# Performance work log

Measured on AMD Instinct MI355X. Metric: run time of the kernel, lower is better.

Reference implementation:

```python
import jax, jax.numpy as jnp
import numpy as np

DIM = 1024
HEADS = 16
HEAD_DIM = DIM // HEADS
MAX_REL = 1024
B, N = 4, 1024


def setup_inputs() -> dict:
    key = jax.random.key(0)
    k1, k2, k3, k4, k5 = jax.random.split(key, 5)
    x = jax.random.normal(k1, (B, N, DIM), dtype=jnp.float32)
    W_qkv = jax.random.normal(k2, (3 * DIM, DIM), dtype=jnp.float32) * 0.02
    W_proj = jax.random.normal(k3, (DIM, DIM), dtype=jnp.float32) * 0.02
    b_proj = jnp.zeros((DIM,), dtype=jnp.float32)
    Er = jax.random.normal(k4, (MAX_REL, HEAD_DIM), dtype=jnp.float32)
    return {"x": x, "W_qkv": W_qkv, "W_proj": W_proj, "b_proj": b_proj, "Er": Er}


def _relative_skew(S_rel):
    # S_rel: [B, H, L, L] -> pad a zero column on the left, reshape, drop first row
    Bb, H, L, _ = S_rel.shape
    S = jnp.pad(S_rel, ((0, 0), (0, 0), (0, 0), (1, 0)))  # [B,H,L,L+1]
    S = S.reshape(Bb, H, L + 1, L)
    return S[:, :, 1:, :]


def reference(x, W_qkv, W_proj, b_proj, Er):
    Bb, Nn, C = x.shape
    scale = HEAD_DIM ** (-0.5)
    qkv = jnp.einsum('bnc,fc->bnf', x, W_qkv)           # [B,N,3C]
    qkv = qkv.reshape(Bb, Nn, 3, HEADS, HEAD_DIM)
    q = jnp.transpose(qkv[:, :, 0], (0, 2, 1, 3))        # [B,H,N,d]
    k = jnp.transpose(qkv[:, :, 1], (0, 2, 1, 3))
    v = jnp.transpose(qkv[:, :, 2], (0, 2, 1, 3))
    content = jnp.einsum('bhnd,bhmd->bhnm', q, k)        # [B,H,N,N]
    er_seq = Er[:Nn]                                     # [N,d]
    rel = jnp.einsum('bhnd,md->bhnm', q, er_seq)         # [B,H,N,N]
    rel = _relative_skew(rel)
    score = (content + rel) * scale
    causal = jnp.triu(jnp.ones((Nn, Nn), dtype=bool), k=1)
    score = jnp.where(causal, -jnp.inf, score)
    probs = jax.nn.softmax(score, axis=-1)
    out = jnp.einsum('bhnm,bhmd->bhnd', probs, v)        # [B,H,N,d]
    out = jnp.transpose(out, (0, 2, 1, 3)).reshape(Bb, Nn, C)
    return jnp.einsum('bnc,oc->bno', out, W_proj) + b_proj
```

## Files before the change

### kernel.cpp

```cpp
#include <hip/hip_runtime.h>
#include <math.h>

#define BATCH 4
#define SEQ   1024
#define DIM_C 1024
#define HEADS 16
#define HDIM  64
#define F3    3072

typedef short bf8 __attribute__((ext_vector_type(8)));
typedef float f32x4 __attribute__((ext_vector_type(4)));

__device__ __forceinline__ ushort f2bf(float f) {
    union { float f; unsigned u; } c; c.f = f;
    unsigned u = c.u + 0x7fffu + ((c.u >> 16) & 1u);
    return (ushort)(u >> 16);
}
__device__ __forceinline__ float bf2f(ushort s) {
    union { unsigned u; float f; } c; c.u = ((unsigned)s) << 16;
    return c.f;
}

__device__ __forceinline__ void stage16(const ushort* g, ushort* l) {
    __builtin_amdgcn_global_load_lds(
        (const __attribute__((address_space(1))) unsigned int*)g,
        (__attribute__((address_space(3))) unsigned int*)l, 16, 0, 0);
}

__global__ __launch_bounds__(256) void cvt_all_kernel(
    const float* __restrict__ x, const float* __restrict__ wqkv,
    const float* __restrict__ wproj, const float* __restrict__ er,
    ushort* __restrict__ xb, ushort* __restrict__ wqkvb,
    ushort* __restrict__ wprojb, ushort* __restrict__ erb)
{
    const int blk = blockIdx.x;
    const float* src; ushort* dst; size_t off;
    if (blk < 2048)      { src = x;     dst = xb;     off = (size_t)blk * 2048; }
    else if (blk < 3584) { src = wqkv;  dst = wqkvb;  off = (size_t)(blk - 2048) * 2048; }
    else if (blk < 4096) { src = wproj; dst = wprojb; off = (size_t)(blk - 3584) * 2048; }
    else                 { src = er;    dst = erb;    off = (size_t)(blk - 4096) * 2048; }
    size_t i = off + (size_t)threadIdx.x * 8;
    float4 v0 = *(const float4*)&src[i];
    float4 v1 = *(const float4*)&src[i + 4];
    ushort o[8];
    o[0] = f2bf(v0.x); o[1] = f2bf(v0.y); o[2] = f2bf(v0.z); o[3] = f2bf(v0.w);
    o[4] = f2bf(v1.x); o[5] = f2bf(v1.y); o[6] = f2bf(v1.z); o[7] = f2bf(v1.w);
    *(uint4*)&dst[i] = *(uint4*)o;
}

__device__ __forceinline__ void gemm_core(
    const ushort* __restrict__ a, const ushort* __restrict__ b,
    ushort* As, ushort* Bs, int m0, int f0, int t, f32x4 (&acc)[4][4])
{
    const int lane = t & 63, w = t >> 6;
    const int lc = lane & 15, g4 = lane >> 4;
    const int wm = (w >> 1) * 64, wn = (w & 1) * 64;
    const int rowS = w * 32 + (lane >> 2);
    const int kkS  = (lane & 3) * 8;

    for (int kt = 0; kt < 32; ++kt) {
        const int k0 = kt * 32;
        __syncthreads();
        #pragma unroll
        for (int ii = 0; ii < 2; ++ii) {
            stage16(&a[(size_t)(m0 + rowS + ii * 16) * 1024 + k0 + kkS],
                    &As[(w * 2 + ii) * 512]);
            stage16(&b[(size_t)(f0 + rowS + ii * 16) * 1024 + k0 + kkS],
                    &Bs[(w * 2 + ii) * 512]);
        }
        __syncthreads();
        bf8 af[4], bfr[4];
        #pragma unroll
        for (int mb = 0; mb < 4; ++mb)
            af[mb] = *(const bf8*)&As[(wm + mb * 16 + lc) * 32 + g4 * 8];
        #pragma unroll
        for (int nb = 0; nb < 4; ++nb)
            bfr[nb] = *(const bf8*)&Bs[(wn + nb * 16 + lc) * 32 + g4 * 8];
        #pragma unroll
        for (int mb = 0; mb < 4; ++mb)
            #pragma unroll
            for (int nb = 0; nb < 4; ++nb)
                acc[mb][nb] = __builtin_amdgcn_mfma_f32_16x16x32_bf16(
                    af[mb], bfr[nb], acc[mb][nb], 0, 0, 0);
    }
}

__global__ __launch_bounds__(256) void gemm_qkv_mfma(
    const ushort* __restrict__ xb, const ushort* __restrict__ wb,
    ushort* __restrict__ qp, ushort* __restrict__ kp, ushort* __restrict__ vp)
{
    __shared__ __align__(16) ushort As[128 * 32];
    __shared__ __align__(16) ushort Bs[128 * 32];
    const int t = threadIdx.x;
    const int m0 = blockIdx.y * 128, f0 = blockIdx.x * 128;
    f32x4 acc[4][4];
    #pragma unroll
    for (int mb = 0; mb < 4; ++mb)
        #pragma unroll
        for (int nb = 0; nb < 4; ++nb) acc[mb][nb] = (f32x4){0.f, 0.f, 0.f, 0.f};

    gemm_core(xb, wb, As, Bs, m0, f0, t, acc);

    const int lane = t & 63, w = t >> 6;
    const int lc = lane & 15, g4 = lane >> 4;
    const int wm = (w >> 1) * 64, wn = (w & 1) * 64;
    const int s = f0 >> 10;
    #pragma unroll
    for (int mb = 0; mb < 4; ++mb)
        #pragma unroll
        for (int nb = 0; nb < 4; ++nb) {
            const int f = f0 + wn + nb * 16 + lc;
            const int h = (f >> 6) & 15, d = f & 63;
            if (s == 2) {
                const int m = m0 + wm + mb * 16 + g4 * 4;
                const int b = m >> 10, n = m & 1023;
                ushort4 o;
                o.x = f2bf(acc[mb][nb][0]); o.y = f2bf(acc[mb][nb][1]);
                o.z = f2bf(acc[mb][nb][2]); o.w = f2bf(acc[mb][nb][3]);
                *(ushort4*)&vp[(((size_t)(b * 16 + h)) * 64 + d) * 1024 + n] = o;
            } else {
                ushort* dst = (s == 0) ? qp : kp;
                #pragma unroll
                for (int i = 0; i < 4; ++i) {
                    const int m = m0 + wm + mb * 16 + g4 * 4 + i;
                    const int b = m >> 10, n = m & 1023;
                    dst[(((size_t)(b * 16 + h)) * 1024 + n) * 64 + d] = f2bf(acc[mb][nb][i]);
                }
            }
        }
}

__global__ __launch_bounds__(256) void gemm_proj_mfma(
    const ushort* __restrict__ ab, const ushort* __restrict__ wb,
    const float* __restrict__ bias, float* __restrict__ y)
{
    __shared__ __align__(16) ushort As[128 * 32];
    __shared__ __align__(16) ushort Bs[128 * 32];
    const int t = threadIdx.x;
    const int m0 = blockIdx.y * 128, f0 = blockIdx.x * 128;
    f32x4 acc[4][4];
    #pragma unroll
    for (int mb = 0; mb < 4; ++mb)
        #pragma unroll
        for (int nb = 0; nb < 4; ++nb) acc[mb][nb] = (f32x4){0.f, 0.f, 0.f, 0.f};

    gemm_core(ab, wb, As, Bs, m0, f0, t, acc);

    const int lane = t & 63, w = t >> 6;
    const int lc = lane & 15, g4 = lane >> 4;
    const int wm = (w >> 1) * 64, wn = (w & 1) * 64;
    #pragma unroll
    for (int mb = 0; mb < 4; ++mb)
        #pragma unroll
        for (int nb = 0; nb < 4; ++nb) {
            const int f = f0 + wn + nb * 16 + lc;
            const float bv = bias[f];
            #pragma unroll
            for (int i = 0; i < 4; ++i) {
                const int m = m0 + wm + mb * 16 + g4 * 4 + i;
                y[(size_t)m * 1024 + f] = acc[mb][nb][i] + bv;
            }
        }
}

__global__ __launch_bounds__(256, 2) void attn_mfma_kernel(
    const ushort* __restrict__ qg, const ushort* __restrict__ kg,
    const ushort* __restrict__ vtg, const ushort* __restrict__ erg,
    ushort* __restrict__ pOd, float* __restrict__ pL)
{
    __shared__ __align__(16) ushort k_s[2][64][64];
    __shared__ __align__(16) ushort vt_s[2][64][64];
    __shared__ __align__(16) ushort e_s[3][64][64];
    __shared__ __align__(16) ushort p_s[4][16][72];

    const int t = threadIdx.x;
    const int w = t >> 6, lane = t & 63;
    const int lc = lane & 15, g4 = lane >> 4;
    const int b = blockIdx.z, h = blockIdx.y;
    const int u = blockIdx.x;
    const int cum[17] = {0,1,2,3,4,6,8,10,12,15,18,21,24,28,32,36,40};
    int bx = 0;
    #pragma unroll
    for (int j = 1; j < 16; ++j) if (u >= cum[j]) bx = j;
    const int part = u - cum[bx];
    const int t0 = part * 4;
    const int t1 = min(t0 + 4, bx + 1);

    const int n0 = bx * 64;
    const int n0w = n0 + w * 16;
    const int ew0 = 48 - 16 * w;
    const int ch0 = 15 - bx + t0;

    const ushort* qb  = qg  + ((size_t)(b * 16 + h)) * 65536;
    const ushort* kb  = kg  + ((size_t)(b * 16 + h)) * 65536;
    const ushort* vtb = vtg + ((size_t)(b * 16 + h)) * 65536;

    const int srow = lane >> 3;
    const int scol = ((lane & 7) ^ (srow & 7)) * 8;
    const int sr0  = w * 16 + srow;
    const int rsw  = (lc & 7) * 8;

    #pragma unroll
    for (int ii = 0; ii < 2; ++ii) {
        stage16(&kb[(size_t)(t0 * 64 + sr0 + ii * 8) * 64 + scol], &k_s[0][w * 16 + ii * 8][0]);
        stage16(&vtb[(size_t)(sr0 + ii * 8) * 1024 + t0 * 64 + scol], &vt_s[0][w * 16 + ii * 8][0]);
    }
    #pragma unroll
    for (int cc = 0; cc < 2; ++cc) {
        const int ch = ch0 + cc;
        #pragma unroll
        for (int ii = 0; ii < 2; ++ii) {
            int gr = ch * 64 + sr0 + ii * 8;
            gr = (gr > 1023) ? 1023 : gr;
            stage16(&erg[(size_t)gr * 64 + scol], &e_s[ch % 3][w * 16 + ii * 8][0]);
        }
    }

    bf8 qf[2];
    #pragma unroll
    for (int c = 0; c < 2; ++c)
        qf[c] = *(const bf8*)&qb[(size_t)(n0w + lc) * 64 + c * 32 + g4 * 8];

    asm volatile("s_waitcnt vmcnt(0)" ::: "memory");
    __builtin_amdgcn_s_barrier();

    const f32x4 z4 = {0.f, 0.f, 0.f, 0.f};
    f32x4 od[4] = {z4, z4, z4, z4};
    float lrow[4] = {0.f, 0.f, 0.f, 0.f};
    int cur = 0;

    for (int tt = t0; tt < t1; ++tt) {
        const int m0 = tt * 64;
        const int ch = 15 - bx + tt;
        const int eB = ch * 64;

        if (tt + 1 < t1) {
            const int m1 = m0 + 64;
            const int nxt = cur ^ 1;
            #pragma unroll
            for (int ii = 0; ii < 2; ++ii) {
                stage16(&kb[(size_t)(m1 + sr0 + ii * 8) * 64 + scol],
                        &k_s[nxt][w * 16 + ii * 8][0]);
                stage16(&vtb[(size_t)(sr0 + ii * 8) * 1024 + m1 + scol],
                        &vt_s[nxt][w * 16 + ii * 8][0]);
            }
            #pragma unroll
            for (int ii = 0; ii < 2; ++ii) {
                int gr = (ch + 2) * 64 + sr0 + ii * 8;
                gr = (gr > 1023) ? 1023 : gr;
                stage16(&erg[(size_t)gr * 64 + scol], &e_s[(ch + 2) % 3][w * 16 + ii * 8][0]);
            }
            asm volatile("s_waitcnt vmcnt(6)" ::: "memory");
        } else {
            asm volatile("s_waitcnt vmcnt(0)" ::: "memory");
        }
        __builtin_amdgcn_s_barrier();

        f32x4 sc[4] = {z4, z4, z4, z4};
        #pragma unroll
        for (int jt = 0; jt < 4; ++jt)
            #pragma unroll
            for (int c = 0; c < 2; ++c) {
                bf8 kf = *(const bf8*)&k_s[cur][jt * 16 + lc][((c * 4 + g4) * 8) ^ rsw];
                sc[jt] = __builtin_amdgcn_mfma_f32_16x16x32_bf16(qf[c], kf, sc[jt], 0, 0, 0);
            }

        f32x4 rc[5] = {z4, z4, z4, z4, z4};
        #pragma unroll
        for (int jr = 0; jr < 5; ++jr) {
            const int g  = eB + ew0 + jr * 16 + lc;
            const int s3 = (g >> 6) % 3;
            const int r  = g & 63;
            #pragma unroll
            for (int c = 0; c < 2; ++c) {
                bf8 ef = *(const bf8*)&e_s[s3][r][((c * 4 + g4) * 8) ^ rsw];
                rc[jr] = __builtin_amdgcn_mfma_f32_16x16x32_bf16(qf[c], ef, rc[jr], 0, 0, 0);
            }
        }

        #pragma unroll
        for (int i = 0; i < 4; ++i) {
            const int row = g4 * 4 + i;
            const int n = n0w + row;
            const int src = (lc + 15 - row) & 15;
            float sh[5];
            #pragma unroll
            for (int jr = 0; jr < 5; ++jr)
                sh[jr] = __shfl(rc[jr][i], src, 16);
            #pragma unroll
            for (int jt = 0; jt < 4; ++jt) {
                const float rel = (lc > row) ? sh[jt + 1] : sh[jt];
                const float s = (sc[jt][i] + rel) * 0.125f;
                const int m = m0 + jt * 16 + lc;
                const float p = (m <= n) ? __expf(s) : 0.f;
                p_s[w][row][jt * 16 + lc] = f2bf(p);
                lrow[i] += p;
            }
        }
        asm volatile("s_waitcnt lgkmcnt(0)" ::: "memory");

        bf8 pf[2];
        #pragma unroll
        for (int c = 0; c < 2; ++c)
            pf[c] = *(const bf8*)&p_s[w][lc][c * 32 + g4 * 8];
        #pragma unroll
        for (int dt = 0; dt < 4; ++dt)
            #pragma unroll
            for (int c = 0; c < 2; ++c) {
                bf8 vf = *(const bf8*)&vt_s[cur][dt * 16 + lc][((c * 4 + g4) * 8) ^ rsw];
                od[dt] = __builtin_amdgcn_mfma_f32_16x16x32_bf16(pf[c], vf, od[dt], 0, 0, 0);
            }

        __builtin_amdgcn_s_barrier();
        cur ^= 1;
    }

    #pragma unroll
    for (int off = 1; off < 16; off <<= 1)
        #pragma unroll
        for (int i = 0; i < 4; ++i)
            lrow[i] += __shfl_xor(lrow[i], off, 16);

    const size_t pbase = (size_t)((b * 16 + h) * 40 + u);
    #pragma unroll
    for (int i = 0; i < 4; ++i) {
        const int nl = w * 16 + g4 * 4 + i;
        #pragma unroll
        for (int dt = 0; dt < 4; ++dt)
            pOd[pbase * 4096 + nl * 64 + dt * 16 + lc] = f2bf(od[dt][i]);
        if (lc == 0) pL[pbase * 64 + nl] = lrow[i];
    }
}

__global__ __launch_bounds__(256) void attn_combine_kernel(
    const ushort* __restrict__ pOd, const float* __restrict__ pL,
    ushort* __restrict__ attnb)
{
    const int tid = blockIdx.x * 256 + threadIdx.x;
    const int d8 = tid & 7;
    const int n  = (tid >> 3) & 1023;
    const int bh = tid >> 13;
    const int bx = n >> 6, nl = n & 63;
    const int cum[17] = {0,1,2,3,4,6,8,10,12,15,18,21,24,28,32,36,40};
    const int u0 = cum[bx], pc = cum[bx + 1] - cum[bx];

    float acc[8] = {0.f, 0.f, 0.f, 0.f, 0.f, 0.f, 0.f, 0.f};
    float lsum = 0.f;
    for (int j = 0; j < pc; ++j) {
        const size_t base = (size_t)(bh * 40 + u0 + j);
        uint4 pv = *(const uint4*)&pOd[base * 4096 + nl * 64 + d8 * 8];
        const ushort* pp = (const ushort*)&pv;
        #pragma unroll
        for (int e = 0; e < 8; ++e) acc[e] += bf2f(pp[e]);
        lsum += pL[base * 64 + nl];
    }
    const float inv = 1.f / lsum;
    ushort o[8];
    #pragma unroll
    for (int e = 0; e < 8; ++e) o[e] = f2bf(acc[e] * inv);
    const int b = bh >> 4, h = bh & 15;
    *(uint4*)&attnb[((size_t)(b * 1024) + n) * 1024 + h * 64 + d8 * 8] = *(uint4*)o;
}

extern "C" void kernel_launch(void* const* d_in, const int* in_sizes, int n_in,
                              void* d_out, int out_size, void* d_ws, size_t ws_size,
                              hipStream_t stream)
{
    const float* x     = (const float*)d_in[0];
    const float* Wqkv  = (const float*)d_in[1];
    const float* Wproj = (const float*)d_in[2];
    const float* bproj = (const float*)d_in[3];
    const float* Er    = (const float*)d_in[4];
    float* out = (float*)d_out;

    const size_t per = (size_t)BATCH * HEADS * SEQ * HDIM;
    ushort* xb     = (ushort*)d_ws;
    ushort* wqkvb  = xb + (size_t)4194304;
    ushort* wprojb = wqkvb + (size_t)3145728;
    ushort* erb    = wprojb + (size_t)1048576;
    ushort* qw     = erb + (size_t)65536;
    ushort* kw     = qw + per;
    ushort* vw     = kw + per;
    ushort* attnb  = vw + per;
    ushort* pOd    = attnb + per;
    float*  pL     = (float*)(pOd + (size_t)64 * 40 * 4096);

    cvt_all_kernel<<<dim3(4128), 256, 0, stream>>>(
        x, Wqkv, Wproj, Er, xb, wqkvb, wprojb, erb);

    gemm_qkv_mfma<<<dim3(F3 / 128, (BATCH * SEQ) / 128), 256, 0, stream>>>(
        xb, wqkvb, qw, kw, vw);

    attn_mfma_kernel<<<dim3(40, HEADS, BATCH), 256, 0, stream>>>(
        qw, kw, vw, erb, pOd, pL);

    attn_combine_kernel<<<dim3(2048), 256, 0, stream>>>(pOd, pL, attnb);

    gemm_proj_mfma<<<dim3(DIM_C / 128, (BATCH * SEQ) / 128), 256, 0, stream>>>(
        attnb, wprojb, bproj, out);
}
```

Before: 199.0 us.

## Use 128-row query tiles with 8 waves per attention block sharing K/V/Er

```diff
diff --git a/kernel.cpp b/kernel.cpp
--- a/kernel.cpp
+++ b/kernel.cpp
@@ -163,57 +163,50 @@
         }
 }
 
-__global__ __launch_bounds__(256, 2) void attn_mfma_kernel(
+__global__ __launch_bounds__(512, 4) void attn_mfma_kernel(
     const ushort* __restrict__ qg, const ushort* __restrict__ kg,
     const ushort* __restrict__ vtg, const ushort* __restrict__ erg,
     ushort* __restrict__ pOd, float* __restrict__ pL)
 {
     __shared__ __align__(16) ushort k_s[2][64][64];
     __shared__ __align__(16) ushort vt_s[2][64][64];
-    __shared__ __align__(16) ushort e_s[3][64][64];
-    __shared__ __align__(16) ushort p_s[4][16][72];
+    __shared__ __align__(16) ushort e_s[4][64][64];
+    __shared__ __align__(16) ushort p_s[8][16][64];
 
     const int t = threadIdx.x;
     const int w = t >> 6, lane = t & 63;
     const int lc = lane & 15, g4 = lane >> 4;
     const int b = blockIdx.z, h = blockIdx.y;
     const int u = blockIdx.x;
-    const int cum[17] = {0,1,2,3,4,6,8,10,12,15,18,21,24,28,32,36,40};
+    const int cum[9] = {0, 1, 2, 4, 6, 9, 12, 16, 20};
     int bx = 0;
     #pragma unroll
-    for (int j = 1; j < 16; ++j) if (u >= cum[j]) bx = j;
+    for (int j = 1; j < 8; ++j) if (u >= cum[j]) bx = j;
     const int part = u - cum[bx];
     const int t0 = part * 4;
-    const int t1 = min(t0 + 4, bx + 1);
-
-    const int n0 = bx * 64;
+    const int t1 = min(t0 + 4, 2 * bx + 2);
+
+    const int n0 = bx * 128;
     const int n0w = n0 + w * 16;
-    const int ew0 = 48 - 16 * w;
-    const int ch0 = 15 - bx + t0;
+    const int ch0 = 14 + t0 - 2 * bx;
 
     const ushort* qb  = qg  + ((size_t)(b * 16 + h)) * 65536;
     const ushort* kb  = kg  + ((size_t)(b * 16 + h)) * 65536;
     const ushort* vtb = vtg + ((size_t)(b * 16 + h)) * 65536;
 
     const int srow = lane >> 3;
-    const int scol = ((lane & 7) ^ (srow & 7)) * 8;
-    const int sr0  = w * 16 + srow;
+    const int scol = ((lane & 7) ^ srow) * 8;
+    const int sr0  = w * 8 + srow;
     const int rsw  = (lc & 7) * 8;
 
-    #pragma unroll
-    for (int ii = 0; ii < 2; ++ii) {
-        stage16(&kb[(size_t)(t0 * 64 + sr0 + ii * 8) * 64 + scol], &k_s[0][w * 16 + ii * 8][0]);
-        stage16(&vtb[(size_t)(sr0 + ii * 8) * 1024 + t0 * 64 + scol], &vt_s[0][w * 16 + ii * 8][0]);
-    }
-    #pragma unroll
-    for (int cc = 0; cc < 2; ++cc) {
+    stage16(&kb[(size_t)(t0 * 64 + sr0) * 64 + scol], &k_s[0][w * 8][0]);
+    stage16(&vtb[(size_t)sr0 * 1024 + t0 * 64 + scol], &vt_s[0][w * 8][0]);
+    #pragma unroll
+    for (int cc = 0; cc < 3; ++cc) {
         const int ch = ch0 + cc;
-        #pragma unroll
-        for (int ii = 0; ii < 2; ++ii) {
-            int gr = ch * 64 + sr0 + ii * 8;
-            gr = (gr > 1023) ? 1023 : gr;
-            stage16(&erg[(size_t)gr * 64 + scol], &e_s[ch % 3][w * 16 + ii * 8][0]);
-        }
+        int gr = ch * 64 + sr0;
+        gr = (gr > 1023) ? 1023 : gr;
+        stage16(&erg[(size_t)gr * 64 + scol], &e_s[ch & 3][w * 8][0]);
     }
 
     bf8 qf[2];
@@ -231,26 +224,17 @@
 
     for (int tt = t0; tt < t1; ++tt) {
         const int m0 = tt * 64;
-        const int ch = 15 - bx + tt;
-        const int eB = ch * 64;
 
         if (tt + 1 < t1) {
             const int m1 = m0 + 64;
             const int nxt = cur ^ 1;
-            #pragma unroll
-            for (int ii = 0; ii < 2; ++ii) {
-                stage16(&kb[(size_t)(m1 + sr0 + ii * 8) * 64 + scol],
-                        &k_s[nxt][w * 16 + ii * 8][0]);
-                stage16(&vtb[(size_t)(sr0 + ii * 8) * 1024 + m1 + scol],
-                        &vt_s[nxt][w * 16 + ii * 8][0]);
-            }
-            #pragma unroll
-            for (int ii = 0; ii < 2; ++ii) {
-                int gr = (ch + 2) * 64 + sr0 + ii * 8;
-                gr = (gr > 1023) ? 1023 : gr;
-                stage16(&erg[(size_t)gr * 64 + scol], &e_s[(ch + 2) % 3][w * 16 + ii * 8][0]);
-            }
-            asm volatile("s_waitcnt vmcnt(6)" ::: "memory");
+            stage16(&kb[(size_t)(m1 + sr0) * 64 + scol], &k_s[nxt][w * 8][0]);
+            stage16(&vtb[(size_t)sr0 * 1024 + m1 + scol], &vt_s[nxt][w * 8][0]);
+            const int chN = 17 + tt - 2 * bx;
+            int gr = chN * 64 + sr0;
+            gr = (gr > 1023) ? 1023 : gr;
+            stage16(&erg[(size_t)gr * 64 + scol], &e_s[chN & 3][w * 8][0]);
+            asm volatile("s_waitcnt vmcnt(3)" ::: "memory");
         } else {
             asm volatile("s_waitcnt vmcnt(0)" ::: "memory");
         }
@@ -265,11 +249,12 @@
                 sc[jt] = __builtin_amdgcn_mfma_f32_16x16x32_bf16(qf[c], kf, sc[jt], 0, 0, 0);
             }
 
+        const int eBw = 1008 + m0 - n0 - 16 * w;
         f32x4 rc[5] = {z4, z4, z4, z4, z4};
         #pragma unroll
         for (int jr = 0; jr < 5; ++jr) {
-            const int g  = eB + ew0 + jr * 16 + lc;
-            const int s3 = (g >> 6) % 3;
+            const int g  = eBw + jr * 16 + lc;
+            const int s3 = (g >> 6) & 3;
             const int r  = g & 63;
             #pragma unroll
             for (int c = 0; c < 2; ++c) {
@@ -293,7 +278,8 @@
                 const float s = (sc[jt][i] + rel) * 0.125f;
                 const int m = m0 + jt * 16 + lc;
                 const float p = (m <= n) ? __expf(s) : 0.f;
-                p_s[w][row][jt * 16 + lc] = f2bf(p);
+                const int blk = (jt * 2 + (lc >> 3)) ^ (row & 7);
+                p_s[w][row][blk * 8 + (lc & 7)] = f2bf(p);
                 lrow[i] += p;
             }
         }
@@ -302,7 +288,7 @@
         bf8 pf[2];
         #pragma unroll
         for (int c = 0; c < 2; ++c)
-            pf[c] = *(const bf8*)&p_s[w][lc][c * 32 + g4 * 8];
+            pf[c] = *(const bf8*)&p_s[w][lc][((c * 4 + g4) ^ (lc & 7)) * 8];
         #pragma unroll
         for (int dt = 0; dt < 4; ++dt)
             #pragma unroll
@@ -321,14 +307,14 @@
         for (int i = 0; i < 4; ++i)
             lrow[i] += __shfl_xor(lrow[i], off, 16);
 
-    const size_t pbase = (size_t)((b * 16 + h) * 40 + u);
+    const size_t pbase = (size_t)((b * 16 + h) * 20 + u);
     #pragma unroll
     for (int i = 0; i < 4; ++i) {
         const int nl = w * 16 + g4 * 4 + i;
         #pragma unroll
         for (int dt = 0; dt < 4; ++dt)
-            pOd[pbase * 4096 + nl * 64 + dt * 16 + lc] = f2bf(od[dt][i]);
-        if (lc == 0) pL[pbase * 64 + nl] = lrow[i];
+            pOd[pbase * 8192 + nl * 64 + dt * 16 + lc] = f2bf(od[dt][i]);
+        if (lc == 0) pL[pbase * 128 + nl] = lrow[i];
     }
 }
 
@@ -340,19 +326,19 @@
     const int d8 = tid & 7;
     const int n  = (tid >> 3) & 1023;
     const int bh = tid >> 13;
-    const int bx = n >> 6, nl = n & 63;
-    const int cum[17] = {0,1,2,3,4,6,8,10,12,15,18,21,24,28,32,36,40};
+    const int bx = n >> 7, nl = n & 127;
+    const int cum[9] = {0, 1, 2, 4, 6, 9, 12, 16, 20};
     const int u0 = cum[bx], pc = cum[bx + 1] - cum[bx];
 
     float acc[8] = {0.f, 0.f, 0.f, 0.f, 0.f, 0.f, 0.f, 0.f};
     float lsum = 0.f;
     for (int j = 0; j < pc; ++j) {
-        const size_t base = (size_t)(bh * 40 + u0 + j);
-        uint4 pv = *(const uint4*)&pOd[base * 4096 + nl * 64 + d8 * 8];
+        const size_t base = (size_t)(bh * 20 + u0 + j);
+        uint4 pv = *(const uint4*)&pOd[base * 8192 + nl * 64 + d8 * 8];
         const ushort* pp = (const ushort*)&pv;
         #pragma unroll
         for (int e = 0; e < 8; ++e) acc[e] += bf2f(pp[e]);
-        lsum += pL[base * 64 + nl];
+        lsum += pL[base * 128 + nl];
     }
     const float inv = 1.f / lsum;
     ushort o[8];
@@ -383,7 +369,7 @@
     ushort* vw     = kw + per;
     ushort* attnb  = vw + per;
     ushort* pOd    = attnb + per;
-    float*  pL     = (float*)(pOd + (size_t)64 * 40 * 4096);
+    float*  pL     = (float*)(pOd + (size_t)64 * 20 * 8192);
 
     cvt_all_kernel<<<dim3(4128), 256, 0, stream>>>(
         x, Wqkv, Wproj, Er, xb, wqkvb, wprojb, erb);
@@ -391,7 +377,7 @@
     gemm_qkv_mfma<<<dim3(F3 / 128, (BATCH * SEQ) / 128), 256, 0, stream>>>(
         xb, wqkvb, qw, kw, vw);
 
-    attn_mfma_kernel<<<dim3(40, HEADS, BATCH), 256, 0, stream>>>(
+    attn_mfma_kernel<<<dim3(20, HEADS, BATCH), 512, 0, stream>>>(
         qw, kw, vw, erb, pOd, pL);
 
     attn_combine_kernel<<<dim3(2048), 256, 0, stream>>>(pOd, pL, attnb);
```

New measurement: 186.9 us, median of 3. 1.06x faster.
